# Kernel optimization log

Hardware: AMD Instinct MI355X
Metric: run time of the kernel (lower is better)

## Reference

```python
import jax, jax.numpy as jnp
import numpy as np

N = 20000      # nodes
E = 320000     # edges (avg degree 16)
HID = 128      # hidden_channel
OUT = 128      # output_channel
SEQ = 8


def setup_inputs() -> dict:
    key = jax.random.key(0)
    ks = jax.random.split(key, 8)
    h = jax.random.normal(ks[0], (N, HID), jnp.float32)
    c = jax.random.normal(ks[1], (N, HID), jnp.float32)
    edge_index = jax.random.randint(ks[2], (2, E), 0, N, jnp.int64)
    edge_attr = jax.random.uniform(ks[3], (E,), jnp.float32)
    # GCNConv weights (PyG: x @ W then propagate), xavier-ish scale
    W_init = jax.random.normal(ks[4], (2 * HID, 2 * OUT), jnp.float32) * (2.0 / (2 * HID + 2 * OUT)) ** 0.5
    b_init = jnp.zeros((2 * OUT,), jnp.float32)
    W_cell = jax.random.normal(ks[5], (HID + OUT, 4 * OUT), jnp.float32) * (2.0 / (HID + OUT + 4 * OUT)) ** 0.5
    b_cell = jnp.zeros((4 * OUT,), jnp.float32)
    return {"h": h, "c": c, "edge_index": edge_index, "edge_attr": edge_attr,
            "W_init": W_init, "b_init": b_init, "W_cell": W_cell, "b_cell": b_cell,
            "seq_len": SEQ}


def _gcn(x, W, b, src, dst, ew, dinv):
    # PyG GCNConv with normalize=True, add_self_loops=True (self-loop weight 1.0)
    xw = x @ W                                   # [N, C_out]
    norm = dinv[src] * ew * dinv[dst]            # sym-normalized edge weights
    agg = jnp.zeros_like(xw).at[dst].add(xw[src] * norm[:, None])
    agg = agg + xw * (dinv * dinv)[:, None]      # self-loop term
    return agg + b


def reference(h, c, edge_index, edge_attr, W_init, b_init, W_cell, b_cell, seq_len):
    src, dst = edge_index[0], edge_index[1]
    n = h.shape[0]
    # degree with self-loops (weight 1.0), shared by both convs
    deg = jnp.zeros((n,), h.dtype).at[dst].add(edge_attr) + 1.0
    dinv = jax.lax.rsqrt(deg)

    # _init_states
    states = jax.nn.elu(_gcn(jnp.concatenate([h, c], axis=1), W_init, b_init, src, dst, edge_attr, dinv))
    h_t, c_t = states[:, :OUT], states[:, OUT:]

    def step(carry, _):
        h_cur, c_cur = carry
        # NOTE: original code feeds the initial h (not h_cur) as x each step
        combined = jnp.concatenate([h, h_cur], axis=1)
        cc = _gcn(combined, W_cell, b_cell, src, dst, edge_attr, dinv)
        cc_i, cc_f, cc_o, cc_g = jnp.split(cc, 4, axis=1)
        c_next = jax.nn.sigmoid(cc_f) * c_cur + jax.nn.sigmoid(cc_i) * jnp.tanh(cc_g)
        h_next = jax.nn.sigmoid(cc_o) * jnp.tanh(c_next)
        return (h_next, c_next), h_next

    (_, _), out = jax.lax.scan(step, (h_t, c_t), None, length=seq_len)
    return out  # [seq_len, N, OUT]
```

## Files before the change

kernel.cpp:

```cpp
#include <hip/hip_runtime.h>

#define N_NODES 20000
#define N_EDGES 320000
#define SEQ 8

typedef __attribute__((ext_vector_type(8))) short bf16x8;
typedef __attribute__((ext_vector_type(4))) float floatx4;
typedef const unsigned int __attribute__((address_space(1)))* gas_u32;
typedef unsigned int __attribute__((address_space(3)))* las_u32;

__device__ __forceinline__ unsigned short f2bf(float f) {
  unsigned int u = __builtin_bit_cast(unsigned int, f);
  return (unsigned short)((u + 0x7fffu + ((u >> 16) & 1u)) >> 16);
}
__device__ __forceinline__ float bflo(unsigned int u) {
  return __builtin_bit_cast(float, u << 16);
}
__device__ __forceinline__ float bfhi(unsigned int u) {
  return __builtin_bit_cast(float, u & 0xffff0000u);
}
__device__ __forceinline__ float sigf(float x) { return 1.f / (1.f + __expf(-x)); }

__device__ __forceinline__ void gl_lds16(const void* g, void* l) {
  auto gp = (gas_u32)g;
  auto lp = (las_u32)(unsigned int)(unsigned long long)l;
  __builtin_amdgcn_global_load_lds(gp, lp, 16, 0, 0);
}


__global__ void k_prologue(const float* __restrict__ Wi,
                           const float* __restrict__ Wc,
                           const float* __restrict__ bc,
                           unsigned short* __restrict__ WiT,
                           unsigned short* __restrict__ W1T,
                           unsigned short* __restrict__ W2T,
                           float* __restrict__ bcp,
                           float* __restrict__ deg, int* __restrict__ counts) {
  int idx = blockIdx.x * 256 + threadIdx.x;
  if (idx < N_NODES) { deg[idx] = 1.0f; counts[idx] = 0; }
  if (idx < 65536) {
    int n = idx >> 8, k = idx & 255;
    WiT[n * 256 + k] = f2bf(Wi[k * 256 + n]);
  }
  if (idx < 512) bcp[idx] = bc[((idx & 3) << 7) | (idx >> 2)];
  int n2 = idx >> 8, k2 = idx & 255;
  if (k2 < 128) {
    int orig = ((n2 & 3) << 7) | (n2 >> 2);
    W1T[n2 * 128 + k2] = f2bf(Wc[k2 * 512 + orig]);
    W2T[n2 * 128 + k2] = f2bf(Wc[(k2 + 128) * 512 + orig]);
  }
}

__global__ void k_deg(const int* __restrict__ ei, const float* __restrict__ ea,
                      float* __restrict__ deg, int* __restrict__ counts) {
  int e = blockIdx.x * 256 + threadIdx.x;
  if (e >= N_EDGES) return;
  int d = ei[N_EDGES + e];
  atomicAdd(&deg[d], ea[e]);
  atomicAdd(&counts[d], 1);
}

__global__ __launch_bounds__(1024) void k_scan(
    const int* __restrict__ counts, const float* __restrict__ deg,
    float* __restrict__ dinv, int* __restrict__ row_ptr,
    int* __restrict__ cursor) {
  __shared__ int sm[1024];
  int t = threadIdx.x;
  int base = t * 20;
  int local[20];
  int s = 0;
#pragma unroll
  for (int i = 0; i < 20; ++i) {
    int g = base + i;
    int v = (g < N_NODES) ? counts[g] : 0;
    local[i] = v;
    s += v;
  }
  sm[t] = s;
  __syncthreads();
  for (int o = 1; o < 1024; o <<= 1) {
    int add = (t >= o) ? sm[t - o] : 0;
    __syncthreads();
    sm[t] += add;
    __syncthreads();
  }
  int run = sm[t] - s;
#pragma unroll
  for (int i = 0; i < 20; ++i) {
    int g = base + i;
    if (g < N_NODES) {
      row_ptr[g] = run;
      cursor[g] = run;
      dinv[g] = rsqrtf(deg[g]);
    }
    run += local[i];
  }
  if (t == 0) row_ptr[N_NODES] = N_EDGES;
}

__global__ void k_fill(const int* __restrict__ ei, const float* __restrict__ ea,
                       const float* __restrict__ dinv, int* __restrict__ cursor,
                       int* __restrict__ csr_src, float* __restrict__ csr_w) {
  int e = blockIdx.x * 256 + threadIdx.x;
  if (e >= N_EDGES) return;
  int s = ei[e], d = ei[N_EDGES + e];
  int k = atomicAdd(&cursor[d], 1);
  csr_src[k] = s;
  csr_w[k] = dinv[s] * ea[e] * dinv[d];
}


__global__ __launch_bounds__(256) void k_agg_init(
    const float* __restrict__ h, const float* __restrict__ c,
    unsigned int* __restrict__ AhAc_u, const float* __restrict__ dinv,
    const int* __restrict__ row_ptr, const int* __restrict__ csr_src,
    const float* __restrict__ csr_w) {
  int wid = (blockIdx.x * 256 + threadIdx.x) >> 6;
  int lane = threadIdx.x & 63;
  if (wid >= N_NODES) return;
  float di = dinv[wid], dd = di * di;
  const float4* xb = (lane < 32) ? (const float4*)h : (const float4*)c;
  int lcol = lane & 31;
  float4 a = xb[(size_t)wid * 32 + lcol];
  float s0 = a.x * dd, s1 = a.y * dd, s2 = a.z * dd, s3 = a.w * dd;
  int e0 = row_ptr[wid], end = row_ptr[wid + 1];
  for (int base = e0; base < end; base += 64) {
    int n = end - base;
    if (n > 64) n = 64;
    int sl = 0;
    float wl = 0.f;
    if (base + lane < end) {
      sl = csr_src[base + lane];
      wl = csr_w[base + lane];
    }
    int j = 0;
    for (; j + 4 <= n; j += 4) {
      int sa = __shfl(sl, j), sb = __shfl(sl, j + 1);
      int sc = __shfl(sl, j + 2), sd = __shfl(sl, j + 3);
      float wa = __shfl(wl, j), wb = __shfl(wl, j + 1);
      float wc = __shfl(wl, j + 2), wd = __shfl(wl, j + 3);
      float4 va = xb[(size_t)sa * 32 + lcol];
      float4 vb = xb[(size_t)sb * 32 + lcol];
      float4 vc = xb[(size_t)sc * 32 + lcol];
      float4 vd = xb[(size_t)sd * 32 + lcol];
      s0 += va.x * wa; s1 += va.y * wa; s2 += va.z * wa; s3 += va.w * wa;
      s0 += vb.x * wb; s1 += vb.y * wb; s2 += vb.z * wb; s3 += vb.w * wb;
      s0 += vc.x * wc; s1 += vc.y * wc; s2 += vc.z * wc; s3 += vc.w * wc;
      s0 += vd.x * wd; s1 += vd.y * wd; s2 += vd.z * wd; s3 += vd.w * wd;
    }
    for (; j < n; ++j) {
      int sa = __shfl(sl, j);
      float wa = __shfl(wl, j);
      float4 va = xb[(size_t)sa * 32 + lcol];
      s0 += va.x * wa; s1 += va.y * wa; s2 += va.z * wa; s3 += va.w * wa;
    }
  }
  uint2 o;
  o.x = (unsigned int)f2bf(s0) | ((unsigned int)f2bf(s1) << 16);
  o.y = (unsigned int)f2bf(s2) | ((unsigned int)f2bf(s3) << 16);
  ((uint2*)AhAc_u)[(size_t)wid * 64 + lane] = o;
}

__global__ __launch_bounds__(256) void k_agg_step(
    const unsigned int* __restrict__ hbf_u, unsigned int* __restrict__ Aht_u,
    const float* __restrict__ dinv, const int* __restrict__ row_ptr,
    const int* __restrict__ csr_src, const float* __restrict__ csr_w) {
  int wid = (blockIdx.x * 256 + threadIdx.x) >> 6;
  int lane = threadIdx.x & 63;
  if (wid >= N_NODES) return;
  float di = dinv[wid], dd = di * di;
  unsigned int a = hbf_u[(size_t)wid * 64 + lane];
  float s0 = bflo(a) * dd, s1 = bfhi(a) * dd;
  int e0 = row_ptr[wid], end = row_ptr[wid + 1];
  for (int base = e0; base < end; base += 64) {
    int n = end - base;
    if (n > 64) n = 64;
    int sl = 0;
    float wl = 0.f;
    if (base + lane < end) {
      sl = csr_src[base + lane];
      wl = csr_w[base + lane];
    }
    int j = 0;
    for (; j + 4 <= n; j += 4) {
      int sa = __shfl(sl, j), sb = __shfl(sl, j + 1);
      int sc = __shfl(sl, j + 2), sd = __shfl(sl, j + 3);
      float wa = __shfl(wl, j), wb = __shfl(wl, j + 1);
      float wc = __shfl(wl, j + 2), wd = __shfl(wl, j + 3);
      unsigned int va = hbf_u[(size_t)sa * 64 + lane];
      unsigned int vb = hbf_u[(size_t)sb * 64 + lane];
      unsigned int vc = hbf_u[(size_t)sc * 64 + lane];
      unsigned int vd = hbf_u[(size_t)sd * 64 + lane];
      s0 += bflo(va) * wa; s1 += bfhi(va) * wa;
      s0 += bflo(vb) * wb; s1 += bfhi(vb) * wb;
      s0 += bflo(vc) * wc; s1 += bfhi(vc) * wc;
      s0 += bflo(vd) * wd; s1 += bfhi(vd) * wd;
    }
    for (; j < n; ++j) {
      int sa = __shfl(sl, j);
      float wa = __shfl(wl, j);
      unsigned int va = hbf_u[(size_t)sa * 64 + lane];
      s0 += bflo(va) * wa; s1 += bfhi(va) * wa;
    }
  }
  Aht_u[(size_t)wid * 64 + lane] =
      (unsigned int)f2bf(s0) | ((unsigned int)f2bf(s1) << 16);
}

template <int EPI, int KK, int LDA>
__global__ __launch_bounds__(256) void k_gemm(
    const unsigned short* __restrict__ A, const unsigned short* __restrict__ BT,
    const float* __restrict__ bias, const float* __restrict__ Kbuf,
    float* __restrict__ c_cur, unsigned short* __restrict__ hbf,
    float* __restrict__ out0) {
  __shared__ __align__(16) union {
    struct { unsigned short a[128 * 64]; unsigned short b[128 * 64]; } ab;
    float ep[64 * 132];
  } sm;
  const int M = N_NODES;
  int tid = threadIdx.x;
  int bm0 = blockIdx.x * 128, bn0 = blockIdx.y * 128;
  int wave = tid >> 6, lane = tid & 63;
  int wrow = (wave >> 1) * 64, wcol = (wave & 1) * 64;
  int lr = lane & 15, lq = lane >> 4;
  int key = lr & 7;

  int lr8 = lane >> 3, cq = lane & 7;
  int gq8 = (cq ^ lr8) * 8;

  floatx4 acc[4][4];
#pragma unroll
  for (int i = 0; i < 4; i++)
#pragma unroll
    for (int j = 0; j < 4; j++) acc[i][j] = (floatx4){0.f, 0.f, 0.f, 0.f};

  for (int k0 = 0; k0 < KK; k0 += 64) {
    __syncthreads();
#pragma unroll
    for (int p = 0; p < 4; ++p) {
      int row = p * 32 + wave * 8;
      int ra = bm0 + row + lr8;
      if (ra > M - 1) ra = M - 1;
      gl_lds16(A + (size_t)ra * LDA + k0 + gq8, sm.ab.a + row * 64);
      gl_lds16(BT + (size_t)(bn0 + row + lr8) * KK + k0 + gq8,
               sm.ab.b + row * 64);
    }
    __syncthreads();
#pragma unroll
    for (int ks = 0; ks < 2; ++ks) {
      int q = ks * 4 + lq;
      int slot = (q ^ key) << 3;
      bf16x8 af[4], bfr[4];
#pragma unroll
      for (int mi = 0; mi < 4; mi++)
        af[mi] = *(const bf16x8*)(sm.ab.a + (wrow + mi * 16 + lr) * 64 + slot);
#pragma unroll
      for (int ni = 0; ni < 4; ni++)
        bfr[ni] = *(const bf16x8*)(sm.ab.b + (wcol + ni * 16 + lr) * 64 + slot);
#pragma unroll
      for (int mi = 0; mi < 4; mi++)
#pragma unroll
        for (int ni = 0; ni < 4; ni++)
          acc[mi][ni] = __builtin_amdgcn_mfma_f32_16x16x32_bf16(
              af[mi], bfr[ni], acc[mi][ni], 0, 0, 0);
    }
  }
  __syncthreads();

  if (EPI == 0) {
#pragma unroll
    for (int mi = 0; mi < 4; mi++) {
#pragma unroll
      for (int r = 0; r < 4; r++) {
        int grow = bm0 + wrow + mi * 16 + lq * 4 + r;
        if (grow >= M) continue;
#pragma unroll
        for (int ni = 0; ni < 4; ni++) {
          int gcol = bn0 + wcol + ni * 16 + lr;
          float v = acc[mi][ni][r] + bias[gcol];
          v = (v > 0.f) ? v : expm1f(v);
          if (gcol < 128) hbf[(size_t)grow * 128 + gcol] = f2bf(v);
          else c_cur[(size_t)grow * 128 + gcol - 128] = v;
        }
      }
    }
  } else if (EPI == 1) {
#pragma unroll
    for (int mi = 0; mi < 4; mi++) {
#pragma unroll
      for (int r = 0; r < 4; r++) {
        int grow = bm0 + wrow + mi * 16 + lq * 4 + r;
        if (grow >= M) continue;
#pragma unroll
        for (int ni = 0; ni < 4; ni++) {
          int gcol = bn0 + wcol + ni * 16 + lr;
          out0[(size_t)grow * 512 + gcol] = acc[mi][ni][r] + bias[gcol];
        }
      }
    }
  } else {
#pragma unroll
    for (int hch = 0; hch < 2; ++hch) {
      if ((wrow >> 6) == hch) {
#pragma unroll
        for (int mi = 0; mi < 4; mi++)
#pragma unroll
          for (int r = 0; r < 4; r++) {
            int row_l = mi * 16 + lq * 4 + r;
#pragma unroll
            for (int ni = 0; ni < 4; ni++)
              sm.ep[row_l * 132 + wcol + ni * 16 + lr] = acc[mi][ni][r];
          }
      }
      __syncthreads();
#pragma unroll
      for (int it = 0; it < 8; ++it) {
        int p = tid + it * 256;
        int row_l = p >> 5, j = p & 31;
        int grow = bm0 + hch * 64 + row_l;
        if (grow < M) {
          int jg = (bn0 >> 2) + j;
          const float* eb = sm.ep + row_l * 132 + 4 * j;
          float4 kb = *(const float4*)&Kbuf[(size_t)grow * 512 + bn0 + 4 * j];
          float gi = eb[0] + kb.x;
          float gf = eb[1] + kb.y;
          float go = eb[2] + kb.z;
          float gg = eb[3] + kb.w;
          size_t o = (size_t)grow * 128 + jg;
          float cp = c_cur[o];
          float cn = sigf(gf) * cp + sigf(gi) * tanhf(gg);
          float hn = sigf(go) * tanhf(cn);
          c_cur[o] = cn;
          hbf[o] = f2bf(hn);
          out0[o] = hn;
        }
      }
      __syncthreads();
    }
  }
}

extern "C" void kernel_launch(void* const* d_in, const int* in_sizes, int n_in,
                              void* d_out, int out_size, void* d_ws, size_t ws_size,
                              hipStream_t stream) {
  const float* h  = (const float*)d_in[0];
  const float* c  = (const float*)d_in[1];
  const int*   ei = (const int*)d_in[2];
  const float* ea = (const float*)d_in[3];
  const float* Wi = (const float*)d_in[4];
  const float* bi = (const float*)d_in[5];
  const float* Wc = (const float*)d_in[6];
  const float* bc = (const float*)d_in[7];
  float* out = (float*)d_out;

  char* w = (char*)d_ws;
  size_t off = 0;
  auto alloc = [&](size_t bytes) {
    void* p = w + off;
    off += (bytes + 511) & ~(size_t)511;
    return p;
  };
  float* deg           = (float*)alloc(N_NODES * 4);
  float* dinv          = (float*)alloc(N_NODES * 4);
  int* counts          = (int*)alloc(N_NODES * 4);
  int* cursor          = (int*)alloc(N_NODES * 4);
  int* row_ptr         = (int*)alloc((N_NODES + 1) * 4);
  int* csr_src         = (int*)alloc(N_EDGES * 4);
  float* csr_w         = (float*)alloc(N_EDGES * 4);
  unsigned short* WiT  = (unsigned short*)alloc(256 * 256 * 2);
  unsigned short* W1T  = (unsigned short*)alloc(512 * 128 * 2);
  unsigned short* W2T  = (unsigned short*)alloc(512 * 128 * 2);
  float* bcp           = (float*)alloc(512 * 4);
  unsigned short* AhAc = (unsigned short*)alloc((size_t)N_NODES * 256 * 2);
  unsigned short* Aht  = (unsigned short*)alloc((size_t)N_NODES * 128 * 2);
  unsigned short* hbf  = (unsigned short*)alloc((size_t)N_NODES * 128 * 2);
  float* c_cur         = (float*)alloc((size_t)N_NODES * 128 * 4);
  float* Kbuf          = (float*)alloc((size_t)N_NODES * 512 * 4);

  const int NB_E = (N_EDGES + 255) / 256;
  const int NB_AGG = N_NODES * 64 / 256;
  const int MB = (N_NODES + 127) / 128;

  k_prologue<<<512, 256, 0, stream>>>(Wi, Wc, bc, WiT, W1T, W2T, bcp, deg,
                                      counts);
  k_deg<<<NB_E, 256, 0, stream>>>(ei, ea, deg, counts);
  k_scan<<<1, 1024, 0, stream>>>(counts, deg, dinv, row_ptr, cursor);
  k_fill<<<NB_E, 256, 0, stream>>>(ei, ea, dinv, cursor, csr_src, csr_w);

  k_agg_init<<<NB_AGG, 256, 0, stream>>>(h, c, (unsigned int*)AhAc, dinv,
                                         row_ptr, csr_src, csr_w);
  k_gemm<0, 256, 256><<<dim3(MB, 2), 256, 0, stream>>>(
      AhAc, WiT, bi, nullptr, c_cur, hbf, nullptr);
  k_gemm<1, 128, 256><<<dim3(MB, 4), 256, 0, stream>>>(
      AhAc, W1T, bcp, nullptr, nullptr, nullptr, Kbuf);

  for (int t = 0; t < SEQ; ++t) {
    k_agg_step<<<NB_AGG, 256, 0, stream>>>((unsigned int*)hbf,
                                           (unsigned int*)Aht, dinv, row_ptr,
                                           csr_src, csr_w);
    k_gemm<2, 128, 128><<<dim3(MB, 4), 256, 0, stream>>>(
        Aht, W2T, nullptr, Kbuf, c_cur, hbf, out + (size_t)t * N_NODES * 128);
  }
}
```

Baseline: 534.7 us.

## Fuse per-step aggregation with gate GEMM and LSTM epilogue in one kernel

Each recurrent step used to run two kernels: a sparse aggregation that wrote Aht to global memory, then a GEMM with the LSTM epilogue. Now one kernel per step aggregates 64 rows into LDS, then loops over four 128-column passes of W2T with MFMA and applies the LSTM update. The h buffer is ping-ponged between two copies so blocks can read the previous h while others write the next one. This removes a global round trip and a launch per step. In exchange, W2T is reloaded for every 64-row block, and the gather phase and the MFMA phase no longer overlap across kernels.

```diff
diff --git a/kernel.cpp b/kernel.cpp
--- a/kernel.cpp
+++ b/kernel.cpp
@@ -161,61 +161,14 @@
   ((uint2*)AhAc_u)[(size_t)wid * 64 + lane] = o;
 }
 
-__global__ __launch_bounds__(256) void k_agg_step(
-    const unsigned int* __restrict__ hbf_u, unsigned int* __restrict__ Aht_u,
-    const float* __restrict__ dinv, const int* __restrict__ row_ptr,
-    const int* __restrict__ csr_src, const float* __restrict__ csr_w) {
-  int wid = (blockIdx.x * 256 + threadIdx.x) >> 6;
-  int lane = threadIdx.x & 63;
-  if (wid >= N_NODES) return;
-  float di = dinv[wid], dd = di * di;
-  unsigned int a = hbf_u[(size_t)wid * 64 + lane];
-  float s0 = bflo(a) * dd, s1 = bfhi(a) * dd;
-  int e0 = row_ptr[wid], end = row_ptr[wid + 1];
-  for (int base = e0; base < end; base += 64) {
-    int n = end - base;
-    if (n > 64) n = 64;
-    int sl = 0;
-    float wl = 0.f;
-    if (base + lane < end) {
-      sl = csr_src[base + lane];
-      wl = csr_w[base + lane];
-    }
-    int j = 0;
-    for (; j + 4 <= n; j += 4) {
-      int sa = __shfl(sl, j), sb = __shfl(sl, j + 1);
-      int sc = __shfl(sl, j + 2), sd = __shfl(sl, j + 3);
-      float wa = __shfl(wl, j), wb = __shfl(wl, j + 1);
-      float wc = __shfl(wl, j + 2), wd = __shfl(wl, j + 3);
-      unsigned int va = hbf_u[(size_t)sa * 64 + lane];
-      unsigned int vb = hbf_u[(size_t)sb * 64 + lane];
-      unsigned int vc = hbf_u[(size_t)sc * 64 + lane];
-      unsigned int vd = hbf_u[(size_t)sd * 64 + lane];
-      s0 += bflo(va) * wa; s1 += bfhi(va) * wa;
-      s0 += bflo(vb) * wb; s1 += bfhi(vb) * wb;
-      s0 += bflo(vc) * wc; s1 += bfhi(vc) * wc;
-      s0 += bflo(vd) * wd; s1 += bfhi(vd) * wd;
-    }
-    for (; j < n; ++j) {
-      int sa = __shfl(sl, j);
-      float wa = __shfl(wl, j);
-      unsigned int va = hbf_u[(size_t)sa * 64 + lane];
-      s0 += bflo(va) * wa; s1 += bfhi(va) * wa;
-    }
-  }
-  Aht_u[(size_t)wid * 64 + lane] =
-      (unsigned int)f2bf(s0) | ((unsigned int)f2bf(s1) << 16);
-}
-
 template <int EPI, int KK, int LDA>
 __global__ __launch_bounds__(256) void k_gemm(
     const unsigned short* __restrict__ A, const unsigned short* __restrict__ BT,
-    const float* __restrict__ bias, const float* __restrict__ Kbuf,
-    float* __restrict__ c_cur, unsigned short* __restrict__ hbf,
-    float* __restrict__ out0) {
-  __shared__ __align__(16) union {
-    struct { unsigned short a[128 * 64]; unsigned short b[128 * 64]; } ab;
-    float ep[64 * 132];
+    const float* __restrict__ bias, float* __restrict__ c_cur,
+    unsigned short* __restrict__ hbf, float* __restrict__ out0) {
+  __shared__ __align__(16) struct {
+    unsigned short a[128 * 64];
+    unsigned short b[128 * 64];
   } sm;
   const int M = N_NODES;
   int tid = threadIdx.x;
@@ -224,7 +177,6 @@
   int wrow = (wave >> 1) * 64, wcol = (wave & 1) * 64;
   int lr = lane & 15, lq = lane >> 4;
   int key = lr & 7;
-
   int lr8 = lane >> 3, cq = lane & 7;
   int gq8 = (cq ^ lr8) * 8;
 
@@ -241,9 +193,9 @@
       int row = p * 32 + wave * 8;
       int ra = bm0 + row + lr8;
       if (ra > M - 1) ra = M - 1;
-      gl_lds16(A + (size_t)ra * LDA + k0 + gq8, sm.ab.a + row * 64);
+      gl_lds16(A + (size_t)ra * LDA + k0 + gq8, sm.a + row * 64);
       gl_lds16(BT + (size_t)(bn0 + row + lr8) * KK + k0 + gq8,
-               sm.ab.b + row * 64);
+               sm.b + row * 64);
     }
     __syncthreads();
 #pragma unroll
@@ -253,10 +205,10 @@
       bf16x8 af[4], bfr[4];
 #pragma unroll
       for (int mi = 0; mi < 4; mi++)
-        af[mi] = *(const bf16x8*)(sm.ab.a + (wrow + mi * 16 + lr) * 64 + slot);
+        af[mi] = *(const bf16x8*)(sm.a + (wrow + mi * 16 + lr) * 64 + slot);
 #pragma unroll
       for (int ni = 0; ni < 4; ni++)
-        bfr[ni] = *(const bf16x8*)(sm.ab.b + (wcol + ni * 16 + lr) * 64 + slot);
+        bfr[ni] = *(const bf16x8*)(sm.b + (wcol + ni * 16 + lr) * 64 + slot);
 #pragma unroll
       for (int mi = 0; mi < 4; mi++)
 #pragma unroll
@@ -265,77 +217,172 @@
               af[mi], bfr[ni], acc[mi][ni], 0, 0, 0);
     }
   }
-  __syncthreads();
-
-  if (EPI == 0) {
-#pragma unroll
-    for (int mi = 0; mi < 4; mi++) {
-#pragma unroll
-      for (int r = 0; r < 4; r++) {
-        int grow = bm0 + wrow + mi * 16 + lq * 4 + r;
-        if (grow >= M) continue;
-#pragma unroll
-        for (int ni = 0; ni < 4; ni++) {
-          int gcol = bn0 + wcol + ni * 16 + lr;
+
+#pragma unroll
+  for (int mi = 0; mi < 4; mi++) {
+#pragma unroll
+    for (int r = 0; r < 4; r++) {
+      int grow = bm0 + wrow + mi * 16 + lq * 4 + r;
+      if (grow >= M) continue;
+#pragma unroll
+      for (int ni = 0; ni < 4; ni++) {
+        int gcol = bn0 + wcol + ni * 16 + lr;
+        if (EPI == 0) {
           float v = acc[mi][ni][r] + bias[gcol];
           v = (v > 0.f) ? v : expm1f(v);
           if (gcol < 128) hbf[(size_t)grow * 128 + gcol] = f2bf(v);
           else c_cur[(size_t)grow * 128 + gcol - 128] = v;
-        }
-      }
-    }
-  } else if (EPI == 1) {
-#pragma unroll
-    for (int mi = 0; mi < 4; mi++) {
-#pragma unroll
-      for (int r = 0; r < 4; r++) {
-        int grow = bm0 + wrow + mi * 16 + lq * 4 + r;
-        if (grow >= M) continue;
-#pragma unroll
-        for (int ni = 0; ni < 4; ni++) {
-          int gcol = bn0 + wcol + ni * 16 + lr;
+        } else {
           out0[(size_t)grow * 512 + gcol] = acc[mi][ni][r] + bias[gcol];
         }
       }
     }
-  } else {
-#pragma unroll
-    for (int hch = 0; hch < 2; ++hch) {
-      if ((wrow >> 6) == hch) {
+  }
+}
+
+__global__ __launch_bounds__(256, 2) void k_step(
+    const unsigned int* __restrict__ hbf_prev,
+    unsigned short* __restrict__ hbf_next,
+    const unsigned short* __restrict__ W2T, const float* __restrict__ Kbuf,
+    float* __restrict__ c_cur, const float* __restrict__ dinv,
+    const int* __restrict__ row_ptr, const int* __restrict__ csr_src,
+    const float* __restrict__ csr_w, float* __restrict__ out_t) {
+  __shared__ __align__(16) unsigned short sA[64 * 136];
+  __shared__ __align__(16) union {
+    unsigned short b[2][128 * 64];
+    float ep[64 * 132];
+  } sB;
+  int tid = threadIdx.x;
+  int wave = tid >> 6, lane = tid & 63;
+  int bm0 = blockIdx.x * 64;
+
+  for (int i = 0; i < 16; ++i) {
+    int rloc = wave * 16 + i;
+    int wid = bm0 + rloc;
+    unsigned int packed = 0u;
+    if (wid < N_NODES) {
+      float di = dinv[wid], dd = di * di;
+      unsigned int a = hbf_prev[(size_t)wid * 64 + lane];
+      float s0 = bflo(a) * dd, s1 = bfhi(a) * dd;
+      int e0 = row_ptr[wid], end = row_ptr[wid + 1];
+      for (int base = e0; base < end; base += 64) {
+        int n = end - base;
+        if (n > 64) n = 64;
+        int sl = 0;
+        float wl = 0.f;
+        if (base + lane < end) {
+          sl = csr_src[base + lane];
+          wl = csr_w[base + lane];
+        }
+        int j = 0;
+        for (; j + 4 <= n; j += 4) {
+          int sa = __shfl(sl, j), sb = __shfl(sl, j + 1);
+          int sc = __shfl(sl, j + 2), sd = __shfl(sl, j + 3);
+          float wa = __shfl(wl, j), wb = __shfl(wl, j + 1);
+          float wc = __shfl(wl, j + 2), wd = __shfl(wl, j + 3);
+          unsigned int va = hbf_prev[(size_t)sa * 64 + lane];
+          unsigned int vb = hbf_prev[(size_t)sb * 64 + lane];
+          unsigned int vc = hbf_prev[(size_t)sc * 64 + lane];
+          unsigned int vd = hbf_prev[(size_t)sd * 64 + lane];
+          s0 += bflo(va) * wa; s1 += bfhi(va) * wa;
+          s0 += bflo(vb) * wb; s1 += bfhi(vb) * wb;
+          s0 += bflo(vc) * wc; s1 += bfhi(vc) * wc;
+          s0 += bflo(vd) * wd; s1 += bfhi(vd) * wd;
+        }
+        for (; j < n; ++j) {
+          int sa = __shfl(sl, j);
+          float wa = __shfl(wl, j);
+          unsigned int va = hbf_prev[(size_t)sa * 64 + lane];
+          s0 += bflo(va) * wa; s1 += bfhi(va) * wa;
+        }
+      }
+      packed = (unsigned int)f2bf(s0) | ((unsigned int)f2bf(s1) << 16);
+    }
+    *(unsigned int*)(sA + rloc * 136 + lane * 2) = packed;
+  }
+
+  int lr = lane & 15, lq = lane >> 4;
+  int key = lr & 7;
+  int lr8 = lane >> 3, cq = lane & 7;
+  int gq8 = (cq ^ lr8) * 8;
+
+  for (int npass = 0; npass < 4; ++npass) {
+    int bn0 = npass * 128;
+    __syncthreads();
+#pragma unroll
+    for (int half = 0; half < 2; ++half) {
+#pragma unroll
+      for (int p = 0; p < 4; ++p) {
+        int row = p * 32 + wave * 8;
+        gl_lds16(W2T + (size_t)(bn0 + row + lr8) * 128 + half * 64 + gq8,
+                 sB.b[half] + row * 64);
+      }
+    }
+    __syncthreads();
+
+    floatx4 acc[4][2];
+#pragma unroll
+    for (int i = 0; i < 4; i++) {
+      acc[i][0] = (floatx4){0.f, 0.f, 0.f, 0.f};
+      acc[i][1] = (floatx4){0.f, 0.f, 0.f, 0.f};
+    }
+#pragma unroll
+    for (int half = 0; half < 2; ++half) {
+#pragma unroll
+      for (int ks = 0; ks < 2; ++ks) {
+        int q = ks * 4 + lq;
+        int slot = (q ^ key) << 3;
+        int kofs = half * 64 + ks * 32 + lq * 8;
+        bf16x8 af[4], bfr[2];
 #pragma unroll
         for (int mi = 0; mi < 4; mi++)
-#pragma unroll
-          for (int r = 0; r < 4; r++) {
-            int row_l = mi * 16 + lq * 4 + r;
-#pragma unroll
-            for (int ni = 0; ni < 4; ni++)
-              sm.ep[row_l * 132 + wcol + ni * 16 + lr] = acc[mi][ni][r];
-          }
-      }
-      __syncthreads();
-#pragma unroll
-      for (int it = 0; it < 8; ++it) {
-        int p = tid + it * 256;
-        int row_l = p >> 5, j = p & 31;
-        int grow = bm0 + hch * 64 + row_l;
-        if (grow < M) {
-          int jg = (bn0 >> 2) + j;
-          const float* eb = sm.ep + row_l * 132 + 4 * j;
-          float4 kb = *(const float4*)&Kbuf[(size_t)grow * 512 + bn0 + 4 * j];
-          float gi = eb[0] + kb.x;
-          float gf = eb[1] + kb.y;
-          float go = eb[2] + kb.z;
-          float gg = eb[3] + kb.w;
-          size_t o = (size_t)grow * 128 + jg;
-          float cp = c_cur[o];
-          float cn = sigf(gf) * cp + sigf(gi) * tanhf(gg);
-          float hn = sigf(go) * tanhf(cn);
-          c_cur[o] = cn;
-          hbf[o] = f2bf(hn);
-          out0[o] = hn;
-        }
-      }
-      __syncthreads();
+          af[mi] = *(const bf16x8*)(sA + (mi * 16 + lr) * 136 + kofs);
+#pragma unroll
+        for (int ni = 0; ni < 2; ni++)
+          bfr[ni] = *(const bf16x8*)(sB.b[half] +
+                                     (wave * 32 + ni * 16 + lr) * 64 + slot);
+#pragma unroll
+        for (int mi = 0; mi < 4; mi++)
+#pragma unroll
+          for (int ni = 0; ni < 2; ni++)
+            acc[mi][ni] = __builtin_amdgcn_mfma_f32_16x16x32_bf16(
+                af[mi], bfr[ni], acc[mi][ni], 0, 0, 0);
+      }
+    }
+    __syncthreads();
+
+#pragma unroll
+    for (int mi = 0; mi < 4; mi++)
+#pragma unroll
+      for (int r = 0; r < 4; r++) {
+        int row_l = mi * 16 + lq * 4 + r;
+#pragma unroll
+        for (int ni = 0; ni < 2; ni++)
+          sB.ep[row_l * 132 + wave * 32 + ni * 16 + lr] = acc[mi][ni][r];
+      }
+    __syncthreads();
+
+#pragma unroll
+    for (int it = 0; it < 8; ++it) {
+      int p = tid + it * 256;
+      int row_l = p >> 5, j = p & 31;
+      int grow = bm0 + row_l;
+      if (grow < N_NODES) {
+        int jg = npass * 32 + j;
+        const float* eb = sB.ep + row_l * 132 + 4 * j;
+        float4 kb = *(const float4*)&Kbuf[(size_t)grow * 512 + bn0 + 4 * j];
+        float gi = eb[0] + kb.x;
+        float gf = eb[1] + kb.y;
+        float go = eb[2] + kb.z;
+        float gg = eb[3] + kb.w;
+        size_t o = (size_t)grow * 128 + jg;
+        float cp = c_cur[o];
+        float cn = sigf(gf) * cp + sigf(gi) * tanhf(gg);
+        float hn = sigf(go) * tanhf(cn);
+        c_cur[o] = cn;
+        hbf_next[o] = f2bf(hn);
+        out_t[o] = hn;
+      }
     }
   }
 }
@@ -372,14 +419,15 @@
   unsigned short* W2T  = (unsigned short*)alloc(512 * 128 * 2);
   float* bcp           = (float*)alloc(512 * 4);
   unsigned short* AhAc = (unsigned short*)alloc((size_t)N_NODES * 256 * 2);
-  unsigned short* Aht  = (unsigned short*)alloc((size_t)N_NODES * 128 * 2);
-  unsigned short* hbf  = (unsigned short*)alloc((size_t)N_NODES * 128 * 2);
+  unsigned short* hbf0 = (unsigned short*)alloc((size_t)N_NODES * 128 * 2);
+  unsigned short* hbf1 = (unsigned short*)alloc((size_t)N_NODES * 128 * 2);
   float* c_cur         = (float*)alloc((size_t)N_NODES * 128 * 4);
   float* Kbuf          = (float*)alloc((size_t)N_NODES * 512 * 4);
 
   const int NB_E = (N_EDGES + 255) / 256;
   const int NB_AGG = N_NODES * 64 / 256;
   const int MB = (N_NODES + 127) / 128;
+  const int SB = (N_NODES + 63) / 64;
 
   k_prologue<<<512, 256, 0, stream>>>(Wi, Wc, bc, WiT, W1T, W2T, bcp, deg,
                                       counts);
@@ -389,16 +437,16 @@
 
   k_agg_init<<<NB_AGG, 256, 0, stream>>>(h, c, (unsigned int*)AhAc, dinv,
                                          row_ptr, csr_src, csr_w);
-  k_gemm<0, 256, 256><<<dim3(MB, 2), 256, 0, stream>>>(
-      AhAc, WiT, bi, nullptr, c_cur, hbf, nullptr);
-  k_gemm<1, 128, 256><<<dim3(MB, 4), 256, 0, stream>>>(
-      AhAc, W1T, bcp, nullptr, nullptr, nullptr, Kbuf);
-
+  k_gemm<0, 256, 256><<<dim3(MB, 2), 256, 0, stream>>>(AhAc, WiT, bi, c_cur,
+                                                       hbf0, nullptr);
+  k_gemm<1, 128, 256><<<dim3(MB, 4), 256, 0, stream>>>(AhAc, W1T, bcp, nullptr,
+                                                       nullptr, Kbuf);
+
+  unsigned short* hb[2] = {hbf0, hbf1};
   for (int t = 0; t < SEQ; ++t) {
-    k_agg_step<<<NB_AGG, 256, 0, stream>>>((unsigned int*)hbf,
-                                           (unsigned int*)Aht, dinv, row_ptr,
-                                           csr_src, csr_w);
-    k_gemm<2, 128, 128><<<dim3(MB, 4), 256, 0, stream>>>(
-        Aht, W2T, nullptr, Kbuf, c_cur, hbf, out + (size_t)t * N_NODES * 128);
-  }
-}
+    k_step<<<SB, 256, 0, stream>>>((const unsigned int*)hb[t & 1],
+                                   hb[(t + 1) & 1], W2T, Kbuf, c_cur, dinv,
+                                   row_ptr, csr_src, csr_w,
+                                   out + (size_t)t * N_NODES * 128);
+  }
+}
```

Measured after the change: 830.5 us. 1.55x slower.
